# Optimization experiments

Measured on AMD Instinct MI355X. Metric: run time of the kernel, lower is better.

## Reference

```python
import jax, jax.numpy as jnp
import numpy as np

N_NODES = 50000
N_EDGES = 800000
N_GRAPHS = 64
NEG_SLOPE = 0.2
BN_EPS = 1e-5


def gat_layer(x, W, a_src, a_dst, bias, src, dst, heads, ch):
    # x: [N, Fin], W: [Fin, heads*ch], a_src/a_dst: [heads, ch]
    N = x.shape[0]
    h = (x @ W).reshape(N, heads, ch)                      # [N,H,C]
    al_s = jnp.sum(h * a_src, axis=-1)                     # [N,H]
    al_d = jnp.sum(h * a_dst, axis=-1)                     # [N,H]
    e = jax.nn.leaky_relu(al_s[src] + al_d[dst], NEG_SLOPE)  # [E,H]
    # segment softmax over destination node neighborhoods
    m = jax.ops.segment_max(e, dst, num_segments=N)        # [N,H]
    ee = jnp.exp(e - m[dst])
    s = jax.ops.segment_sum(ee, dst, num_segments=N)
    alpha = ee / (s[dst] + 1e-16)                          # [E,H]
    out = jax.ops.segment_sum(alpha[:, :, None] * h[src], dst, num_segments=N)
    return out.reshape(N, heads * ch) + bias


def bn_eval(x, gamma, beta, mean, var):
    return (x - mean) * jax.lax.rsqrt(var + BN_EPS) * gamma + beta


def setup_inputs() -> dict:
    key = jax.random.key(0)
    ks = jax.random.split(key, 32)
    d = {}
    d['x'] = jax.random.normal(ks[0], (N_NODES, 128), dtype=jnp.float32)
    d['edge_index'] = jax.random.randint(ks[1], (2, N_EDGES), 0, N_NODES, dtype=jnp.int32)
    d['batch'] = jnp.sort(jax.random.randint(ks[2], (N_NODES,), 0, N_GRAPHS, dtype=jnp.int32))
    def glorot(k, shape):
        fan = shape[0] + shape[-1]
        return jax.random.normal(k, shape, dtype=jnp.float32) * jnp.sqrt(2.0 / fan)
    # layer 1: 128 -> 8 heads x 32
    d['W1'] = glorot(ks[3], (128, 256)); d['a1s'] = glorot(ks[4], (8, 32)); d['a1d'] = glorot(ks[5], (8, 32)); d['b1'] = jnp.zeros((256,), jnp.float32)
    d['g1'] = jax.random.uniform(ks[6], (256,), jnp.float32, 0.5, 1.5); d['be1'] = jax.random.normal(ks[7], (256,)) * 0.1
    d['m1'] = jax.random.normal(ks[8], (256,)) * 0.1; d['v1'] = jax.random.uniform(ks[9], (256,), jnp.float32, 0.5, 1.5)
    # layer 2: 256 -> 8 heads x 64
    d['W2'] = glorot(ks[10], (256, 512)); d['a2s'] = glorot(ks[11], (8, 64)); d['a2d'] = glorot(ks[12], (8, 64)); d['b2'] = jnp.zeros((512,), jnp.float32)
    d['g2'] = jax.random.uniform(ks[13], (512,), jnp.float32, 0.5, 1.5); d['be2'] = jax.random.normal(ks[14], (512,)) * 0.1
    d['m2'] = jax.random.normal(ks[15], (512,)) * 0.1; d['v2'] = jax.random.uniform(ks[16], (512,), jnp.float32, 0.5, 1.5)
    # layer 3: 512 -> 8 heads x 32
    d['W3'] = glorot(ks[17], (512, 256)); d['a3s'] = glorot(ks[18], (8, 32)); d['a3d'] = glorot(ks[19], (8, 32)); d['b3'] = jnp.zeros((256,), jnp.float32)
    d['g3'] = jax.random.uniform(ks[20], (256,), jnp.float32, 0.5, 1.5); d['be3'] = jax.random.normal(ks[21], (256,)) * 0.1
    d['m3'] = jax.random.normal(ks[22], (256,)) * 0.1; d['v3'] = jax.random.uniform(ks[23], (256,), jnp.float32, 0.5, 1.5)
    # global attention gate + heads
    d['gw'] = glorot(ks[24], (256, 1)); d['gb'] = jnp.zeros((1,), jnp.float32)
    d['f1w'] = glorot(ks[25], (256, 16)); d['f1b'] = jnp.zeros((16,), jnp.float32)
    d['f2w'] = glorot(ks[26], (16, 1)); d['f2b'] = jnp.zeros((1,), jnp.float32)
    return d


def reference(x, edge_index, batch, W1, a1s, a1d, b1, g1, be1, m1, v1,
              W2, a2s, a2d, b2, g2, be2, m2, v2,
              W3, a3s, a3d, b3, g3, be3, m3, v3,
              gw, gb, f1w, f1b, f2w, f2b):
    N = x.shape[0]
    loops = jnp.arange(N, dtype=edge_index.dtype)
    src = jnp.concatenate([edge_index[0], loops])   # add self-loops (PyG default)
    dst = jnp.concatenate([edge_index[1], loops])
    h = jax.nn.relu(bn_eval(gat_layer(x, W1, a1s, a1d, b1, src, dst, 8, 32), g1, be1, m1, v1))
    h = jax.nn.relu(bn_eval(gat_layer(h, W2, a2s, a2d, b2, src, dst, 8, 64), g2, be2, m2, v2))
    h = jax.nn.relu(bn_eval(gat_layer(h, W3, a3s, a3d, b3, src, dst, 8, 32), g3, be3, m3, v3))
    # GlobalAttention pooling: softmax(gate) over each graph, weighted sum
    gate = (h @ gw + gb)                                   # [N,1]
    gm = jax.ops.segment_max(gate, batch, num_segments=N_GRAPHS)
    ge = jnp.exp(gate - gm[batch])
    gs = jax.ops.segment_sum(ge, batch, num_segments=N_GRAPHS)
    w = ge / (gs[batch] + 1e-16)
    pooled = jax.ops.segment_sum(w * h, batch, num_segments=N_GRAPHS)  # [G,256]
    out = jax.nn.relu(pooled @ f1w + f1b)
    return out @ f2w + f2b
```

## Files before the change

### kernel.cpp

```cpp
#include <hip/hip_runtime.h>
#include <cstddef>
#include <cstdint>

typedef unsigned short ushort_t;
typedef __attribute__((ext_vector_type(8))) short short8;
typedef __attribute__((ext_vector_type(4))) short short4v;
typedef __attribute__((ext_vector_type(4))) float f32x4;

__device__ __forceinline__ float bf2f(unsigned short u) {
  union { uint32_t i; float f; } x; x.i = ((uint32_t)u) << 16; return x.f;
}
__device__ __forceinline__ unsigned short f2bf(float f) {
  union { float f; uint32_t i; } x; x.f = f;
  uint32_t u = x.i;
  return (unsigned short)((u + 0x7fffu + ((u >> 16) & 1)) >> 16);
}
__device__ __forceinline__ void acc2(float ee, uint32_t wv, float& a, float& b) {
  a += ee * bf2f((unsigned short)(wv & 0xffffu));
  b += ee * bf2f((unsigned short)(wv >> 16));
}

__global__ void count_kernel(const int* __restrict__ dst, int* __restrict__ cnt,
                             int E, int N) {
  int i = blockIdx.x * blockDim.x + threadIdx.x;
  if (i >= E + N) return;
  int d = (i < E) ? dst[i] : (i - E);
  atomicAdd(&cnt[d], 1);
}

__global__ void scan1_kernel(const int* __restrict__ cnt, int* __restrict__ exc,
                             int* __restrict__ psum, int N) {
  __shared__ int tmp[256];
  int tid = threadIdx.x;
  int i = blockIdx.x * 256 + tid;
  int v = (i < N) ? cnt[i] : 0;
  tmp[tid] = v;
  __syncthreads();
  for (int d = 1; d < 256; d <<= 1) {
    int t = (tid >= d) ? tmp[tid - d] : 0;
    __syncthreads();
    tmp[tid] += t;
    __syncthreads();
  }
  if (i < N) exc[i] = tmp[tid] - v;
  if (tid == 255) psum[blockIdx.x] = tmp[255];
}

__global__ void scan2_kernel(int* __restrict__ psum, int* __restrict__ offs,
                             int nb, int N) {
  __shared__ int tmp[256];
  int tid = threadIdx.x;
  int v = (tid < nb) ? psum[tid] : 0;
  tmp[tid] = v;
  __syncthreads();
  for (int d = 1; d < 256; d <<= 1) {
    int t = (tid >= d) ? tmp[tid - d] : 0;
    __syncthreads();
    tmp[tid] += t;
    __syncthreads();
  }
  if (tid < nb) psum[tid] = tmp[tid] - v;
  if (tid == 255) offs[N] = tmp[255];
}

__global__ void scan3_kernel(const int* __restrict__ exc, const int* __restrict__ psum,
                             int* __restrict__ offs, int* __restrict__ fill, int N) {
  int i = blockIdx.x * blockDim.x + threadIdx.x;
  if (i >= N) return;
  int e = exc[i] + psum[i >> 8];
  offs[i] = e;
  fill[i] = e;
}

__global__ void fill_kernel(const int* __restrict__ src, const int* __restrict__ dst,
                            int* __restrict__ fill, int* __restrict__ srcs,
                            int E, int N) {
  int i = blockIdx.x * blockDim.x + threadIdx.x;
  if (i >= E + N) return;
  int s, d;
  if (i < E) { s = src[i]; d = dst[i]; } else { s = i - E; d = s; }
  int pos = atomicAdd(&fill[d], 1);
  srcs[pos] = s;
}

__global__ void starts_kernel(const int* __restrict__ batch, int* __restrict__ gstart,
                              int N, int G) {
  int n = blockIdx.x * blockDim.x + threadIdx.x;
  if (n >= N) return;
  if (n == 0) {
    int b0 = batch[0];
    for (int g = 0; g <= b0; ++g) gstart[g] = 0;
    int bl = batch[N - 1];
    for (int g = bl + 1; g <= G; ++g) gstart[g] = N;
  } else {
    int a = batch[n - 1], b = batch[n];
    for (int g = a + 1; g <= b; ++g) gstart[g] = n;
  }
}

__global__ void f2bf_kernel(const float* __restrict__ in, unsigned short* __restrict__ out,
                            int n4) {
  int i = blockIdx.x * 256 + threadIdx.x;
  if (i >= n4) return;
  float4 v = *reinterpret_cast<const float4*>(in + (size_t)i * 4);
  unsigned short o[4] = {f2bf(v.x), f2bf(v.y), f2bf(v.z), f2bf(v.w)};
  *reinterpret_cast<uint2*>(out + (size_t)i * 4) = *reinterpret_cast<uint2*>(o);
}

__global__ void wt_kernel(const float* __restrict__ W, unsigned short* __restrict__ WT,
                          int K, int C) {
  int i = blockIdx.x * 256 + threadIdx.x;
  if (i >= K * C) return;
  int c = i / K, k = i - c * K;
  WT[i] = f2bf(W[(size_t)k * C + c]);
}

__global__ void __launch_bounds__(256)
gemm_bf16(const unsigned short* __restrict__ A, const unsigned short* __restrict__ BT,
          unsigned short* __restrict__ C, int M, int K, int Nc) {
  __shared__ unsigned short As[8192];
  __shared__ unsigned short Bs[8192];
  int tid = threadIdx.x;
  int lane = tid & 63;
  int w = tid >> 6;
  int wm = w & 1, wn = w >> 1;
  int m0 = blockIdx.x * 128, n0 = blockIdx.y * 128;
  f32x4 zero = {0.f, 0.f, 0.f, 0.f};
  f32x4 acc[4][4];
#pragma unroll
  for (int i = 0; i < 4; ++i)
#pragma unroll
    for (int j = 0; j < 4; ++j) acc[i][j] = zero;

  for (int k0 = 0; k0 < K; k0 += 64) {
    __syncthreads();
#pragma unroll
    for (int it = 0; it < 4; ++it) {
      int phys = it * 4096 + tid * 16;
      int row = phys >> 7;
      int col16 = ((phys >> 4) & 7) ^ (row & 7);
      int arow = m0 + row; arow = arow < M ? arow : M - 1;
      const unsigned short* ga = A + (size_t)arow * K + k0 + col16 * 8;
      __builtin_amdgcn_global_load_lds(
          (const __attribute__((address_space(1))) void*)ga,
          (__attribute__((address_space(3))) void*)((char*)As + phys), 16, 0, 0);
      const unsigned short* gb = BT + (size_t)(n0 + row) * K + k0 + col16 * 8;
      __builtin_amdgcn_global_load_lds(
          (const __attribute__((address_space(1))) void*)gb,
          (__attribute__((address_space(3))) void*)((char*)Bs + phys), 16, 0, 0);
    }
    asm volatile("s_waitcnt vmcnt(0)" ::: "memory");
    __syncthreads();
#pragma unroll
    for (int ks = 0; ks < 2; ++ks) {
      short8 af[4], bfr[4];
#pragma unroll
      for (int m = 0; m < 4; ++m) {
        int row = wm * 64 + m * 16 + (lane & 15);
        int colb = ks * 64 + (lane >> 4) * 16;
        int phys = (row << 7) + (colb ^ ((row & 7) << 4));
        af[m] = *(const short8*)((const char*)As + phys);
      }
#pragma unroll
      for (int n = 0; n < 4; ++n) {
        int row = wn * 64 + n * 16 + (lane & 15);
        int colb = ks * 64 + (lane >> 4) * 16;
        int phys = (row << 7) + (colb ^ ((row & 7) << 4));
        bfr[n] = *(const short8*)((const char*)Bs + phys);
      }
#pragma unroll
      for (int m = 0; m < 4; ++m)
#pragma unroll
        for (int n = 0; n < 4; ++n)
          acc[m][n] = __builtin_amdgcn_mfma_f32_16x16x32_bf16(af[m], bfr[n], acc[m][n], 0, 0, 0);
    }
  }
#pragma unroll
  for (int m = 0; m < 4; ++m) {
#pragma unroll
    for (int r = 0; r < 4; ++r) {
      int row = m0 + wm * 64 + m * 16 + (lane >> 4) * 4 + r;
      if (row < M) {
#pragma unroll
        for (int n = 0; n < 4; ++n) {
          int col = n0 + wn * 64 + n * 16 + (lane & 15);
          C[(size_t)row * Nc + col] = f2bf(acc[m][n][r]);
        }
      }
    }
  }
}

template <int COUT>
__global__ void __launch_bounds__(256)
al2_kernel(const unsigned short* __restrict__ hpre, const float* __restrict__ a_s,
           const float* __restrict__ a_d, float* __restrict__ als,
           float* __restrict__ ald, int N) {
  constexpr int VEC = COUT / 64;
  int wv = threadIdx.x >> 6;
  int lane = threadIdx.x & 63;
  int n = blockIdx.x * 4 + wv;
  if (n >= N) return;
  const unsigned short* hp = hpre + (size_t)n * COUT + VEC * lane;
  unsigned short h[VEC];
  if (VEC == 4) *reinterpret_cast<short4v*>(h) = *reinterpret_cast<const short4v*>(hp);
  else          *reinterpret_cast<short8*>(h) = *reinterpret_cast<const short8*>(hp);
  float vs = 0.f, vd = 0.f;
#pragma unroll
  for (int v = 0; v < VEC; ++v) {
    float f = bf2f(h[v]);
    vs += f * a_s[VEC * lane + v];
    vd += f * a_d[VEC * lane + v];
  }
  vs += __shfl_xor(vs, 1); vd += __shfl_xor(vd, 1);
  vs += __shfl_xor(vs, 2); vd += __shfl_xor(vd, 2);
  vs += __shfl_xor(vs, 4); vd += __shfl_xor(vd, 4);
  if ((lane & 7) == 0) {
    int hd = lane >> 3;
    als[(size_t)n * 8 + hd] = vs;
    ald[(size_t)n * 8 + hd] = vd;
  }
}

#define LEAKY(x) ((x) >= 0.f ? (x) : 0.2f * (x))
template <int COUT, bool GATE>
__global__ void __launch_bounds__(256)
agg4_kernel(const unsigned short* __restrict__ hpre, const float* __restrict__ als,
            const float* __restrict__ ald, const int* __restrict__ srcs,
            const int* __restrict__ offs, const float* __restrict__ bias,
            const float* __restrict__ gamma, const float* __restrict__ beta,
            const float* __restrict__ mean, const float* __restrict__ var,
            unsigned short* __restrict__ hout,
            const float* __restrict__ gw, const float* __restrict__ gb,
            float* __restrict__ gate, int N) {
  constexpr int VEC = COUT / 64;
  constexpr int CAP = 128;
  constexpr int EPAD = 132;
  __shared__ float ehs[4][8][EPAD];
  __shared__ int srcsS[4][CAP];
  int tid = threadIdx.x;
  int w = tid >> 6, l = tid & 63;
  int n = blockIdx.x * 4 + w;
  if (n >= N) return;
  int e0 = offs[n];
  int deg = offs[n + 1] - e0;
  int mcap = deg < CAP ? deg : CAP;
  int hdA = l & 7;
  int eb = l >> 3;
  float aldv = ald[((size_t)n << 3) + hdA];

  for (int e = l; e < mcap; e += 64) srcsS[w][e] = srcs[e0 + e];

  for (int e = eb; e < mcap; e += 8) {
    int s = srcsS[w][e];
    float xx = als[((size_t)(uint32_t)s << 3) + hdA] + aldv;
    ehs[w][hdA][e] = LEAKY(xx);
  }
  float mx = -1e30f;
  for (int e = eb; e < mcap; e += 8) mx = fmaxf(mx, ehs[w][hdA][e]);
  for (int e = CAP + eb; e < deg; e += 8) {
    int s = srcs[e0 + e];
    mx = fmaxf(mx, LEAKY(als[((size_t)(uint32_t)s << 3) + hdA] + aldv));
  }
  mx = fmaxf(mx, __shfl_xor(mx, 8));
  mx = fmaxf(mx, __shfl_xor(mx, 16));
  mx = fmaxf(mx, __shfl_xor(mx, 32));
  float dp = 0.f;
  for (int e = eb; e < mcap; e += 8) {
    float ee = __expf(ehs[w][hdA][e] - mx);
    ehs[w][hdA][e] = ee;
    dp += ee;
  }
  for (int e = CAP + eb; e < deg; e += 8) {
    int s = srcs[e0 + e];
    dp += __expf(LEAKY(als[((size_t)(uint32_t)s << 3) + hdA] + aldv) - mx);
  }
  dp += __shfl_xor(dp, 8);
  dp += __shfl_xor(dp, 16);
  dp += __shfl_xor(dp, 32);
  float dinv = 1.f / (dp + 1e-16f);

  int hdC = l >> 3;
  float dinvC = __shfl(dinv, hdC);
  float mxC = __shfl(mx, hdC);
  float aldC = __shfl(aldv, hdC);
  const float* eerow = ehs[w][hdC];

  float num[VEC] = {};
  int e = 0;
  if (VEC == 4) {
    const uint2* hp = reinterpret_cast<const uint2*>(hpre);
    for (; e + 4 <= mcap; e += 4) {
      int s0 = srcsS[w][e], s1 = srcsS[w][e + 1];
      int s2 = srcsS[w][e + 2], s3 = srcsS[w][e + 3];
      uint2 w0 = hp[((size_t)(uint32_t)s0 << 6) + l];
      uint2 w1 = hp[((size_t)(uint32_t)s1 << 6) + l];
      uint2 w2 = hp[((size_t)(uint32_t)s2 << 6) + l];
      uint2 w3 = hp[((size_t)(uint32_t)s3 << 6) + l];
      float ee0 = eerow[e], ee1 = eerow[e + 1], ee2 = eerow[e + 2], ee3 = eerow[e + 3];
      acc2(ee0, w0.x, num[0], num[1]); acc2(ee0, w0.y, num[2], num[3]);
      acc2(ee1, w1.x, num[0], num[1]); acc2(ee1, w1.y, num[2], num[3]);
      acc2(ee2, w2.x, num[0], num[1]); acc2(ee2, w2.y, num[2], num[3]);
      acc2(ee3, w3.x, num[0], num[1]); acc2(ee3, w3.y, num[2], num[3]);
    }
    for (; e < mcap; ++e) {
      int s = srcsS[w][e];
      uint2 w0 = hp[((size_t)(uint32_t)s << 6) + l];
      float ee0 = eerow[e];
      acc2(ee0, w0.x, num[0], num[1]); acc2(ee0, w0.y, num[2], num[3]);
    }
    for (; e < deg; ++e) {
      int s = srcs[e0 + e];
      float ee0 = __expf(LEAKY(als[((size_t)(uint32_t)s << 3) + hdC] + aldC) - mxC);
      uint2 w0 = hp[((size_t)(uint32_t)s << 6) + l];
      acc2(ee0, w0.x, num[0], num[1]); acc2(ee0, w0.y, num[2], num[3]);
    }
  } else {
    const uint4* hp = reinterpret_cast<const uint4*>(hpre);
    for (; e + 4 <= mcap; e += 4) {
      int s0 = srcsS[w][e], s1 = srcsS[w][e + 1];
      int s2 = srcsS[w][e + 2], s3 = srcsS[w][e + 3];
      uint4 w0 = hp[((size_t)(uint32_t)s0 << 6) + l];
      uint4 w1 = hp[((size_t)(uint32_t)s1 << 6) + l];
      uint4 w2 = hp[((size_t)(uint32_t)s2 << 6) + l];
      uint4 w3 = hp[((size_t)(uint32_t)s3 << 6) + l];
      float ee0 = eerow[e], ee1 = eerow[e + 1], ee2 = eerow[e + 2], ee3 = eerow[e + 3];
      acc2(ee0, w0.x, num[0], num[1]); acc2(ee0, w0.y, num[2], num[3]);
      acc2(ee0, w0.z, num[4], num[5]); acc2(ee0, w0.w, num[6], num[7]);
      acc2(ee1, w1.x, num[0], num[1]); acc2(ee1, w1.y, num[2], num[3]);
      acc2(ee1, w1.z, num[4], num[5]); acc2(ee1, w1.w, num[6], num[7]);
      acc2(ee2, w2.x, num[0], num[1]); acc2(ee2, w2.y, num[2], num[3]);
      acc2(ee2, w2.z, num[4], num[5]); acc2(ee2, w2.w, num[6], num[7]);
      acc2(ee3, w3.x, num[0], num[1]); acc2(ee3, w3.y, num[2], num[3]);
      acc2(ee3, w3.z, num[4], num[5]); acc2(ee3, w3.w, num[6], num[7]);
    }
    for (; e < mcap; ++e) {
      int s = srcsS[w][e];
      uint4 w0 = hp[((size_t)(uint32_t)s << 6) + l];
      float ee0 = eerow[e];
      acc2(ee0, w0.x, num[0], num[1]); acc2(ee0, w0.y, num[2], num[3]);
      acc2(ee0, w0.z, num[4], num[5]); acc2(ee0, w0.w, num[6], num[7]);
    }
    for (; e < deg; ++e) {
      int s = srcs[e0 + e];
      float ee0 = __expf(LEAKY(als[((size_t)(uint32_t)s << 3) + hdC] + aldC) - mxC);
      uint4 w0 = hp[((size_t)(uint32_t)s << 6) + l];
      acc2(ee0, w0.x, num[0], num[1]); acc2(ee0, w0.y, num[2], num[3]);
      acc2(ee0, w0.z, num[4], num[5]); acc2(ee0, w0.w, num[6], num[7]);
    }
  }

  unsigned short o[VEC];
  float gp = 0.f;
#pragma unroll
  for (int v = 0; v < VEC; ++v) {
    int c = VEC * l + v;
    float xo = num[v] * dinvC + bias[c];
    xo = (xo - mean[c]) * rsqrtf(var[c] + 1e-5f) * gamma[c] + beta[c];
    xo = fmaxf(xo, 0.f);
    o[v] = f2bf(xo);
    if (GATE) gp += xo * gw[c];
  }
  if (VEC == 4)
    *reinterpret_cast<uint2*>(&hout[(size_t)n * COUT + VEC * l]) = *reinterpret_cast<uint2*>(o);
  else
    *reinterpret_cast<uint4*>(&hout[(size_t)n * COUT + VEC * l]) = *reinterpret_cast<uint4*>(o);
  if (GATE) {
    gp += __shfl_xor(gp, 1);
    gp += __shfl_xor(gp, 2);
    gp += __shfl_xor(gp, 4);
    gp += __shfl_xor(gp, 8);
    gp += __shfl_xor(gp, 16);
    gp += __shfl_xor(gp, 32);
    if (l == 0) gate[n] = gp + gb[0];
  }
}

__global__ void __launch_bounds__(256)
poolmax_kernel(const float* __restrict__ gate, const int* __restrict__ gstart,
               float* __restrict__ gmax, float* __restrict__ ginv) {
  int g = blockIdx.x;
  int tid = threadIdx.x;
  int n0 = gstart[g], n1 = gstart[g + 1];
  __shared__ float red[4];
  float mx = -1e30f;
  for (int n = n0 + tid; n < n1; n += 256) mx = fmaxf(mx, gate[n]);
#pragma unroll
  for (int o = 32; o >= 1; o >>= 1) mx = fmaxf(mx, __shfl_xor(mx, o));
  if ((tid & 63) == 0) red[tid >> 6] = mx;
  __syncthreads();
  mx = fmaxf(fmaxf(red[0], red[1]), fmaxf(red[2], red[3]));
  __syncthreads();
  float sm = 0.f;
  for (int n = n0 + tid; n < n1; n += 256) sm += __expf(gate[n] - mx);
#pragma unroll
  for (int o = 32; o >= 1; o >>= 1) sm += __shfl_xor(sm, o);
  if ((tid & 63) == 0) red[tid >> 6] = sm;
  __syncthreads();
  if (tid == 0) {
    sm = red[0] + red[1] + red[2] + red[3];
    gmax[g] = mx;
    ginv[g] = 1.f / (sm + 1e-16f);
  }
}

__global__ void __launch_bounds__(256)
poolsum_kernel(const float* __restrict__ gate, const unsigned short* __restrict__ h3,
               const int* __restrict__ batch, const float* __restrict__ gmax,
               const float* __restrict__ ginv, float* __restrict__ pooled, int N) {
  int tid = threadIdx.x;
  int nbase = blockIdx.x * 64;
  float acc = 0.f;
  int cur = batch[nbase];
  for (int i = 0; i < 64; ++i) {
    int n = nbase + i;
    if (n >= N) break;
    int b = batch[n];
    if (b != cur) {
      atomicAdd(&pooled[cur * 256 + tid], acc);
      acc = 0.f;
      cur = b;
    }
    float w = __expf(gate[n] - gmax[b]) * ginv[b];
    acc += w * bf2f(h3[(size_t)n * 256 + tid]);
  }
  atomicAdd(&pooled[cur * 256 + tid], acc);
}

__global__ void __launch_bounds__(64)
head_kernel(const float* __restrict__ pooled, const float* __restrict__ f1w,
            const float* __restrict__ f1b, const float* __restrict__ f2w,
            const float* __restrict__ f2b, float* __restrict__ out) {
  int g = blockIdx.x;
  int l = threadIdx.x;
  float p[4];
#pragma unroll
  for (int v = 0; v < 4; ++v) p[v] = pooled[g * 256 + l * 4 + v];
  float acc = 0.f;
#pragma unroll
  for (int j = 0; j < 16; ++j) {
    float s = 0.f;
#pragma unroll
    for (int v = 0; v < 4; ++v) s += p[v] * f1w[(l * 4 + v) * 16 + j];
#pragma unroll
    for (int o = 32; o >= 1; o >>= 1) s += __shfl_xor(s, o);
    float hj = fmaxf(s + f1b[j], 0.f);
    acc += hj * f2w[j];
  }
  if (l == 0) out[g] = acc + f2b[0];
}

extern "C" void kernel_launch(void* const* d_in, const int* in_sizes, int n_in,
                              void* d_out, int out_size, void* d_ws, size_t ws_size,
                              hipStream_t stream) {
  const float* x    = (const float*)d_in[0];
  const int*   ei   = (const int*)d_in[1];
  const int*   batch= (const int*)d_in[2];
  const float* W1   = (const float*)d_in[3];
  const float* a1s  = (const float*)d_in[4];
  const float* a1d  = (const float*)d_in[5];
  const float* b1   = (const float*)d_in[6];
  const float* g1   = (const float*)d_in[7];
  const float* be1  = (const float*)d_in[8];
  const float* m1   = (const float*)d_in[9];
  const float* v1   = (const float*)d_in[10];
  const float* W2   = (const float*)d_in[11];
  const float* a2s  = (const float*)d_in[12];
  const float* a2d  = (const float*)d_in[13];
  const float* b2   = (const float*)d_in[14];
  const float* g2   = (const float*)d_in[15];
  const float* be2  = (const float*)d_in[16];
  const float* m2   = (const float*)d_in[17];
  const float* v2   = (const float*)d_in[18];
  const float* W3   = (const float*)d_in[19];
  const float* a3s  = (const float*)d_in[20];
  const float* a3d  = (const float*)d_in[21];
  const float* b3   = (const float*)d_in[22];
  const float* g3   = (const float*)d_in[23];
  const float* be3  = (const float*)d_in[24];
  const float* m3   = (const float*)d_in[25];
  const float* v3   = (const float*)d_in[26];
  const float* gw   = (const float*)d_in[27];
  const float* gb   = (const float*)d_in[28];
  const float* f1w  = (const float*)d_in[29];
  const float* f1b  = (const float*)d_in[30];
  const float* f2w  = (const float*)d_in[31];
  const float* f2b  = (const float*)d_in[32];

  int N = in_sizes[2];
  int E = in_sizes[1] / 2;
  const int* esrc = ei;
  const int* edst = ei + E;

  char* ws = (char*)d_ws;
  size_t off = 0;
  auto take = [&](size_t bytes) -> void* {
    void* p = ws + off;
    off += (bytes + 255) & ~(size_t)255;
    return p;
  };
  unsigned short* XBF  = (unsigned short*)take((size_t)N * 128 * 2);
  unsigned short* WT1  = (unsigned short*)take((size_t)256 * 128 * 2);
  unsigned short* WT2  = (unsigned short*)take((size_t)512 * 256 * 2);
  unsigned short* WT3  = (unsigned short*)take((size_t)256 * 512 * 2);
  unsigned short* HPRE = (unsigned short*)take((size_t)N * 512 * 2);
  unsigned short* HB   = (unsigned short*)take((size_t)N * 512 * 2);
  float* ALS   = (float*)take((size_t)N * 8 * 4);
  float* ALD   = (float*)take((size_t)N * 8 * 4);
  int*   CNT   = (int*)take((size_t)N * 4);
  int*   OFFS  = (int*)take((size_t)(N + 1) * 4);
  int*   FILL  = (int*)take((size_t)N * 4);
  int*   EXC   = (int*)take((size_t)N * 4);
  int*   PSUM  = (int*)take(256 * 4);
  int*   SRCS  = (int*)take((size_t)(E + N) * 4);
  float* GATE  = (float*)take((size_t)N * 4);
  int*   GST   = (int*)take(65 * 4);
  float* POOLED= (float*)take(64 * 256 * 4);
  float* GMAX  = (float*)take(64 * 4);
  float* GINV  = (float*)take(64 * 4);
  (void)ws_size; (void)n_in; (void)out_size;

  f2bf_kernel<<<(N * 128 / 4 + 255) / 256, 256, 0, stream>>>(x, XBF, N * 128 / 4);
  wt_kernel<<<(128 * 256 + 255) / 256, 256, 0, stream>>>(W1, WT1, 128, 256);
  wt_kernel<<<(256 * 512 + 255) / 256, 256, 0, stream>>>(W2, WT2, 256, 512);
  wt_kernel<<<(512 * 256 + 255) / 256, 256, 0, stream>>>(W3, WT3, 512, 256);

  hipMemsetAsync(CNT, 0, (size_t)N * 4, stream);
  hipMemsetAsync(POOLED, 0, 64 * 256 * 4, stream);
  int tE = E + N;
  count_kernel<<<(tE + 255) / 256, 256, 0, stream>>>(edst, CNT, E, N);
  int nb = (N + 255) / 256;
  scan1_kernel<<<nb, 256, 0, stream>>>(CNT, EXC, PSUM, N);
  scan2_kernel<<<1, 256, 0, stream>>>(PSUM, OFFS, nb, N);
  scan3_kernel<<<nb, 256, 0, stream>>>(EXC, PSUM, OFFS, FILL, N);
  fill_kernel<<<(tE + 255) / 256, 256, 0, stream>>>(esrc, edst, FILL, SRCS, E, N);
  starts_kernel<<<(N + 255) / 256, 256, 0, stream>>>(batch, GST, N, 64);

  int mgrid = (N + 127) / 128;
  int agrid = (N + 3) / 4;

  {
    dim3 gg(mgrid, 256 / 128);
    gemm_bf16<<<gg, 256, 0, stream>>>(XBF, WT1, HPRE, N, 128, 256);
    al2_kernel<256><<<agrid, 256, 0, stream>>>(HPRE, a1s, a1d, ALS, ALD, N);
    agg4_kernel<256, false><<<agrid, 256, 0, stream>>>(HPRE, ALS, ALD, SRCS, OFFS,
                                                       b1, g1, be1, m1, v1, HB,
                                                       nullptr, nullptr, nullptr, N);
  }
  {
    dim3 gg(mgrid, 512 / 128);
    gemm_bf16<<<gg, 256, 0, stream>>>(HB, WT2, HPRE, N, 256, 512);
    al2_kernel<512><<<agrid, 256, 0, stream>>>(HPRE, a2s, a2d, ALS, ALD, N);
    agg4_kernel<512, false><<<agrid, 256, 0, stream>>>(HPRE, ALS, ALD, SRCS, OFFS,
                                                       b2, g2, be2, m2, v2, HB,
                                                       nullptr, nullptr, nullptr, N);
  }
  {
    dim3 gg(mgrid, 256 / 128);
    gemm_bf16<<<gg, 256, 0, stream>>>(HB, WT3, HPRE, N, 512, 256);
    al2_kernel<256><<<agrid, 256, 0, stream>>>(HPRE, a3s, a3d, ALS, ALD, N);
    agg4_kernel<256, true><<<agrid, 256, 0, stream>>>(HPRE, ALS, ALD, SRCS, OFFS,
                                                      b3, g3, be3, m3, v3, HB,
                                                      gw, gb, GATE, N);
  }

  poolmax_kernel<<<64, 256, 0, stream>>>(GATE, GST, GMAX, GINV);
  poolsum_kernel<<<(N + 63) / 64, 256, 0, stream>>>(GATE, HB, batch, GMAX, GINV, POOLED, N);
  head_kernel<<<64, 64, 0, stream>>>(POOLED, f1w, f1b, f2w, f2b, (float*)d_out);
}
```

Measured before the change: 512.3 us.

## Merge weight transposes, swizzle GEMM blocks across XCDs, deepen gather unroll

Three separate changes. The three weight-transpose launches are merged into a single kernel to save launch overhead. The GEMM grid becomes one-dimensional, with a block-index swizzle that gives each XCD a contiguous range of tiles so neighbouring tiles share L2. The VEC==4 aggregation loop now issues 8 independent row gathers before accumulating, to raise memory-level parallelism at the cost of more registers.

After: 497.7 us, median of 2. 2.8% less time.

```diff
diff --git a/kernel.cpp b/kernel.cpp
--- a/kernel.cpp
+++ b/kernel.cpp
@@ -107,24 +107,38 @@
   *reinterpret_cast<uint2*>(out + (size_t)i * 4) = *reinterpret_cast<uint2*>(o);
 }
 
-__global__ void wt_kernel(const float* __restrict__ W, unsigned short* __restrict__ WT,
-                          int K, int C) {
+__global__ void wt3_kernel(const float* __restrict__ W1, const float* __restrict__ W2,
+                           const float* __restrict__ W3,
+                           unsigned short* __restrict__ WT1, unsigned short* __restrict__ WT2,
+                           unsigned short* __restrict__ WT3) {
   int i = blockIdx.x * 256 + threadIdx.x;
-  if (i >= K * C) return;
-  int c = i / K, k = i - c * K;
-  WT[i] = f2bf(W[(size_t)k * C + c]);
+  const float* W; unsigned short* WT; int K, C, j;
+  if (i < 32768)       { W = W1; WT = WT1; K = 128; C = 256; j = i; }
+  else if (i < 163840) { W = W2; WT = WT2; K = 256; C = 512; j = i - 32768; }
+  else if (i < 294912) { W = W3; WT = WT3; K = 512; C = 256; j = i - 163840; }
+  else return;
+  int c = j / K, k = j - c * K;
+  WT[j] = f2bf(W[(size_t)k * C + c]);
 }
 
 __global__ void __launch_bounds__(256)
 gemm_bf16(const unsigned short* __restrict__ A, const unsigned short* __restrict__ BT,
-          unsigned short* __restrict__ C, int M, int K, int Nc) {
+          unsigned short* __restrict__ C, int M, int K, int Nc, int yshift) {
   __shared__ unsigned short As[8192];
   __shared__ unsigned short Bs[8192];
+  int nwg = gridDim.x;
+  int q = nwg >> 3, r = nwg & 7;
+  int wg = blockIdx.x;
+  int xcd = wg & 7, idx = wg >> 3;
+  int swz = (xcd < r) ? (xcd * (q + 1) + idx)
+                      : (r * (q + 1) + (xcd - r) * q + idx);
+  int x = swz >> yshift, y = swz & ((1 << yshift) - 1);
+  int m0 = x << 7, n0 = y << 7;
+
   int tid = threadIdx.x;
   int lane = tid & 63;
   int w = tid >> 6;
   int wm = w & 1, wn = w >> 1;
-  int m0 = blockIdx.x * 128, n0 = blockIdx.y * 128;
   f32x4 zero = {0.f, 0.f, 0.f, 0.f};
   f32x4 acc[4][4];
 #pragma unroll
@@ -178,13 +192,13 @@
 #pragma unroll
   for (int m = 0; m < 4; ++m) {
 #pragma unroll
-    for (int r = 0; r < 4; ++r) {
-      int row = m0 + wm * 64 + m * 16 + (lane >> 4) * 4 + r;
+    for (int r2 = 0; r2 < 4; ++r2) {
+      int row = m0 + wm * 64 + m * 16 + (lane >> 4) * 4 + r2;
       if (row < M) {
 #pragma unroll
         for (int n = 0; n < 4; ++n) {
           int col = n0 + wn * 64 + n * 16 + (lane & 15);
-          C[(size_t)row * Nc + col] = f2bf(acc[m][n][r]);
+          C[(size_t)row * Nc + col] = f2bf(acc[m][n][r2]);
         }
       }
     }
@@ -290,18 +304,31 @@
   int e = 0;
   if (VEC == 4) {
     const uint2* hp = reinterpret_cast<const uint2*>(hpre);
+    for (; e + 8 <= mcap; e += 8) {
+      uint2 wv[8];
+#pragma unroll
+      for (int j = 0; j < 8; ++j) {
+        int s = srcsS[w][e + j];
+        wv[j] = hp[((size_t)(uint32_t)s << 6) + l];
+      }
+#pragma unroll
+      for (int j = 0; j < 8; ++j) {
+        float ee = eerow[e + j];
+        acc2(ee, wv[j].x, num[0], num[1]); acc2(ee, wv[j].y, num[2], num[3]);
+      }
+    }
     for (; e + 4 <= mcap; e += 4) {
-      int s0 = srcsS[w][e], s1 = srcsS[w][e + 1];
-      int s2 = srcsS[w][e + 2], s3 = srcsS[w][e + 3];
-      uint2 w0 = hp[((size_t)(uint32_t)s0 << 6) + l];
-      uint2 w1 = hp[((size_t)(uint32_t)s1 << 6) + l];
-      uint2 w2 = hp[((size_t)(uint32_t)s2 << 6) + l];
-      uint2 w3 = hp[((size_t)(uint32_t)s3 << 6) + l];
-      float ee0 = eerow[e], ee1 = eerow[e + 1], ee2 = eerow[e + 2], ee3 = eerow[e + 3];
-      acc2(ee0, w0.x, num[0], num[1]); acc2(ee0, w0.y, num[2], num[3]);
-      acc2(ee1, w1.x, num[0], num[1]); acc2(ee1, w1.y, num[2], num[3]);
-      acc2(ee2, w2.x, num[0], num[1]); acc2(ee2, w2.y, num[2], num[3]);
-      acc2(ee3, w3.x, num[0], num[1]); acc2(ee3, w3.y, num[2], num[3]);
+      uint2 wv[4];
+#pragma unroll
+      for (int j = 0; j < 4; ++j) {
+        int s = srcsS[w][e + j];
+        wv[j] = hp[((size_t)(uint32_t)s << 6) + l];
+      }
+#pragma unroll
+      for (int j = 0; j < 4; ++j) {
+        float ee = eerow[e + j];
+        acc2(ee, wv[j].x, num[0], num[1]); acc2(ee, wv[j].y, num[2], num[3]);
+      }
     }
     for (; e < mcap; ++e) {
       int s = srcsS[w][e];
@@ -521,9 +548,7 @@
   (void)ws_size; (void)n_in; (void)out_size;
 
   f2bf_kernel<<<(N * 128 / 4 + 255) / 256, 256, 0, stream>>>(x, XBF, N * 128 / 4);
-  wt_kernel<<<(128 * 256 + 255) / 256, 256, 0, stream>>>(W1, WT1, 128, 256);
-  wt_kernel<<<(256 * 512 + 255) / 256, 256, 0, stream>>>(W2, WT2, 256, 512);
-  wt_kernel<<<(512 * 256 + 255) / 256, 256, 0, stream>>>(W3, WT3, 512, 256);
+  wt3_kernel<<<(294912 + 255) / 256, 256, 0, stream>>>(W1, W2, W3, WT1, WT2, WT3);
 
   hipMemsetAsync(CNT, 0, (size_t)N * 4, stream);
   hipMemsetAsync(POOLED, 0, 64 * 256 * 4, stream);
@@ -540,24 +565,21 @@
   int agrid = (N + 3) / 4;
 
   {
-    dim3 gg(mgrid, 256 / 128);
-    gemm_bf16<<<gg, 256, 0, stream>>>(XBF, WT1, HPRE, N, 128, 256);
+    gemm_bf16<<<mgrid * 2, 256, 0, stream>>>(XBF, WT1, HPRE, N, 128, 256, 1);
     al2_kernel<256><<<agrid, 256, 0, stream>>>(HPRE, a1s, a1d, ALS, ALD, N);
     agg4_kernel<256, false><<<agrid, 256, 0, stream>>>(HPRE, ALS, ALD, SRCS, OFFS,
                                                        b1, g1, be1, m1, v1, HB,
                                                        nullptr, nullptr, nullptr, N);
   }
   {
-    dim3 gg(mgrid, 512 / 128);
-    gemm_bf16<<<gg, 256, 0, stream>>>(HB, WT2, HPRE, N, 256, 512);
+    gemm_bf16<<<mgrid * 4, 256, 0, stream>>>(HB, WT2, HPRE, N, 256, 512, 2);
     al2_kernel<512><<<agrid, 256, 0, stream>>>(HPRE, a2s, a2d, ALS, ALD, N);
     agg4_kernel<512, false><<<agrid, 256, 0, stream>>>(HPRE, ALS, ALD, SRCS, OFFS,
                                                        b2, g2, be2, m2, v2, HB,
                                                        nullptr, nullptr, nullptr, N);
   }
   {
-    dim3 gg(mgrid, 256 / 128);
-    gemm_bf16<<<gg, 256, 0, stream>>>(HB, WT3, HPRE, N, 512, 256);
+    gemm_bf16<<<mgrid * 2, 256, 0, stream>>>(HB, WT3, HPRE, N, 512, 256, 1);
     al2_kernel<256><<<agrid, 256, 0, stream>>>(HPRE, a3s, a3d, ALS, ALD, N);
     agg4_kernel<256, true><<<agrid, 256, 0, stream>>>(HPRE, ALS, ALD, SRCS, OFFS,
                                                       b3, g3, be3, m3, v3, HB,
```
